# Kernel tuning notes

Hardware: AMD Instinct MI355X
Metric: run time of the kernel (lower is better)

The kernel has to match this reference:

```python
import jax, jax.numpy as jnp
import numpy as np

LN_EPS = 1e-5
ALPHA_Q = 1.0

def _ln(t, g, b):
    mu = jnp.mean(t, -1, keepdims=True)
    var = jnp.var(t, -1, keepdims=True)
    return (t - mu) / jnp.sqrt(var + LN_EPS) * g + b

def _mlp(t, w1, b1, w2, b2):
    h = jax.nn.gelu(t @ w1.T + b1, approximate=False)
    return h @ w2.T + b2

def setup_inputs() -> dict:
    key = jax.random.key(0)
    B, N, L, E, H, D = 2, 2048, 2048, 1024, 16, 4
    ks = jax.random.split(key, 40)
    rn = lambda i, shape, sc: jax.random.normal(ks[i], shape, jnp.float32) * sc
    inp = {}
    inp['x'] = rn(0, (B, N, E), 1.0)
    inp['xp'] = jax.random.uniform(ks[1], (B, N, D), jnp.float32)
    inp['y'] = rn(2, (B, L, E), 1.0)
    inp['yp'] = jax.random.uniform(ks[3], (B, L, D), jnp.float32)
    inp['attn_mask'] = jax.random.uniform(ks[4], (1, 1, N, L), jnp.float32)
    # PositionEncoder params (torch Linear convention: weight [out,in])
    inp['p_w1'] = rn(5, (E, D), 1.0 / D)
    inp['p_b1'] = jax.random.uniform(ks[6], (E,), jnp.float32, 0.0, np.pi)
    inp['p_w2'] = rn(7, (E, D), 1.0 / D)
    inp['p_b2'] = jax.random.uniform(ks[8], (E,), jnp.float32, 0.0, np.pi)
    # QueryEncoder: LayerNorm + mlp1 + mlp2 (mlp0 is dead code in the source)
    inp['q_ln_g'] = jnp.ones((E,), jnp.float32); inp['q_ln_b'] = jnp.zeros((E,), jnp.float32)
    inp['q_m1_w1'] = rn(9, (2 * E, E), 0.02); inp['q_m1_b1'] = jnp.zeros((2 * E,), jnp.float32)
    inp['q_m1_w2'] = rn(10, (E, 2 * E), 0.02); inp['q_m1_b2'] = jnp.zeros((E,), jnp.float32)
    inp['q_m2_w1'] = rn(11, (2 * E, E), 0.02); inp['q_m2_b1'] = jnp.zeros((2 * E,), jnp.float32)
    inp['q_m2_w2'] = rn(12, (E, 2 * E), 0.02); inp['q_m2_b2'] = jnp.zeros((E,), jnp.float32)
    # KeyEncoder: LayerNorm + mlp1 (mlp0 dead code)
    inp['k_ln_g'] = jnp.ones((E,), jnp.float32); inp['k_ln_b'] = jnp.zeros((E,), jnp.float32)
    inp['k_m1_w1'] = rn(13, (2 * E, E), 0.02); inp['k_m1_b1'] = jnp.zeros((2 * E,), jnp.float32)
    inp['k_m1_w2'] = rn(14, (E, 2 * E), 0.02); inp['k_m1_b2'] = jnp.zeros((E,), jnp.float32)
    # V: LayerNorm + Linear
    inp['v_ln_g'] = jnp.ones((E,), jnp.float32); inp['v_ln_b'] = jnp.zeros((E,), jnp.float32)
    inp['v_w'] = rn(15, (E, E), 0.02); inp['v_b'] = jnp.zeros((E,), jnp.float32)
    # output projections
    inp['proj1_w'] = rn(16, (E, E), 0.02); inp['proj1_b'] = jnp.zeros((E,), jnp.float32)
    inp['proj2_w'] = rn(17, (E, D * H), 0.02); inp['proj2_b'] = jnp.zeros((E,), jnp.float32)
    return inp

def reference(x, xp, y, yp, attn_mask, p_w1, p_b1, p_w2, p_b2,
              q_ln_g, q_ln_b, q_m1_w1, q_m1_b1, q_m1_w2, q_m1_b2,
              q_m2_w1, q_m2_b1, q_m2_w2, q_m2_b2,
              k_ln_g, k_ln_b, k_m1_w1, k_m1_b1, k_m1_w2, k_m1_b2,
              v_ln_g, v_ln_b, v_w, v_b, proj1_w, proj1_b, proj2_w, proj2_b):
    B, N, E = x.shape
    L = y.shape[1]
    D = xp.shape[2]
    H = proj2_w.shape[1] // D
    C = E // H
    # PositionEncoder: query side with bias, key side without bias
    pxt = ALPHA_Q * xp
    xp1 = pxt @ p_w1.T + p_b1            # [B,N,E]
    xp2 = pxt @ p_w2.T + p_b2
    pyt = ALPHA_Q * yp
    yp1 = pyt @ p_w1.T                   # [B,L,E], no bias
    yp2 = pyt @ p_w2.T
    rh = lambda t: t.reshape(t.shape[0], -1, H, C)
    # QueryEncoder
    xn = _ln(x, q_ln_g, q_ln_b)
    x1 = _mlp(xn, q_m1_w1, q_m1_b1, q_m1_w2, q_m1_b2)
    x2 = _mlp(xn, q_m2_w1, q_m2_b1, q_m2_w2, q_m2_b2)
    q = jnp.concatenate([rh(x1 * jnp.cos(xp1)), rh(x1 * jnp.sin(xp1)),
                         rh(x2 * jnp.cos(xp2)), rh(x2 * jnp.sin(xp2))], axis=-1)  # [B,N,H,4C]
    # KeyEncoder (note: second cos/sin block is the raw position code)
    yn = _ln(y, k_ln_g, k_ln_b)
    y1 = _mlp(yn, k_m1_w1, k_m1_b1, k_m1_w2, k_m1_b2)
    k = jnp.concatenate([rh(y1 * jnp.cos(yp1)), rh(y1 * jnp.sin(yp1)),
                         rh(jnp.cos(yp2)), rh(jnp.sin(yp2))], axis=-1)            # [B,L,H,4C]
    scale = (4 * C) ** (-0.5)
    attn = jax.nn.softmax(jnp.einsum('bnhd,blhd->bhnl', q, k) * scale, axis=-1)
    # masked renormalization (mask applied AFTER softmax)
    eps = min(1e-8, 1.0 / L)
    attn = attn * attn_mask
    attn = attn / (jnp.sum(attn, axis=-1, keepdims=True) + eps)
    # values
    v = (_ln(y, v_ln_g, v_ln_b) @ v_w.T + v_b).reshape(B, L, H, C)
    out1 = jnp.einsum('bhnl,blhc->bnhc', attn, v).reshape(B, N, E) @ proj1_w.T + proj1_b
    out2 = jnp.einsum('bhnl,bld->bnhd', attn, yp) - xp[:, :, None, :]             # [B,N,H,D]
    out2 = out2.reshape(B, N, H * D) @ proj2_w.T + proj2_b
    return (out1 + out2, attn, xp)
```

## Files before the change

### kernel.cpp

```cpp
#include <hip/hip_runtime.h>
#include <math.h>
#include <stdint.h>

#define DEV static __device__ __forceinline__

typedef __bf16 bf16x8 __attribute__((ext_vector_type(8)));
typedef __bf16 bf16x4v __attribute__((ext_vector_type(4)));
typedef float f32x4 __attribute__((ext_vector_type(4)));

constexpr int Nn = 2048, Ll = 2048, Ee = 1024, Hh = 16;
constexpr float SCALE = 0.0625f;

constexpr size_t OFF_XN   = 0;
constexpr size_t OFF_YNK  = 8388608;
constexpr size_t OFF_YNV  = 16777216;
constexpr size_t OFF_H12  = 25165824;
constexpr size_t OFF_H3   = 58720256;
constexpr size_t OFF_X1   = 75497472;
constexpr size_t OFF_X2   = 83886080;
constexpr size_t OFF_Y1   = 92274688;
constexpr size_t OFF_QWS  = 100663296;
constexpr size_t OFF_KWS  = 134217728;
constexpr size_t OFF_VWS  = 167772160;
constexpr size_t OFF_DNV  = 176160768;
constexpr size_t OFF_YPT  = 176422912;
constexpr size_t OFF_MSK  = 176685056;
constexpr size_t OFF_AVZ  = 185073664;
constexpr size_t OFF_W1122= 193986560;
constexpr size_t OFF_W12  = 202375168;
constexpr size_t OFF_W22  = 206569472;
constexpr size_t OFF_WK1  = 210763776;
constexpr size_t OFF_WK2  = 214958080;
constexpr size_t OFF_WV   = 219152384;
constexpr size_t OFF_WP   = 221249536;
constexpr size_t OFF_EM   = 223477760;

DEV void gl2l(const void* g, void* l) {
  __builtin_amdgcn_global_load_lds((const __attribute__((address_space(1))) void*)g,
                                   (__attribute__((address_space(3))) void*)l, 16, 0, 0);
}

DEV float gelu_f(float v) {
  float x = v * 0.70710678118654752f;
  float ax = fabsf(x);
  float t = 1.f / fmaf(0.3275911f, ax, 1.f);
  float y = t * fmaf(t, fmaf(t, fmaf(t, fmaf(t, 1.061405429f, -1.453152027f),
                                     1.421413741f), -0.284496736f), 0.254829592f);
  float er = 1.f - y * __expf(-x * x);
  er = (x < 0.f) ? -er : er;
  return 0.5f * v * (1.f + er);
}

__launch_bounds__(256)
__global__ void prep_all(const float* __restrict__ s0, const float* __restrict__ s1,
                         const float* __restrict__ s2, const float* __restrict__ s3,
                         const float* __restrict__ s4, const float* __restrict__ s5,
                         const float* __restrict__ s6,
                         __bf16* __restrict__ d0, __bf16* __restrict__ d1,
                         __bf16* __restrict__ d2, __bf16* __restrict__ d3,
                         __bf16* __restrict__ d4, __bf16* __restrict__ d5,
                         __bf16* __restrict__ d6,
                         const float* __restrict__ pw1, const float* __restrict__ pw2,
                         __bf16* __restrict__ wp,
                         const float* __restrict__ mask, __bf16* __restrict__ mb,
                         const float* __restrict__ yp, __bf16* __restrict__ ypT) {
  int u = blockIdx.x * 256 + threadIdx.x;
  if (u < 3407872) {
    int seg = u >> 19, r = u & 524287;
    const float* s; __bf16* d;
    if      (seg == 0) { s = s0; d = d0; }
    else if (seg == 1) { s = s1; d = d1; }
    else if (seg == 2) { s = s2; d = d2; }
    else if (seg == 3) { s = s3; d = d3; }
    else if (seg == 4) { s = s4; d = d4; }
    else if (seg == 5) { s = s5; d = d5; }
    else               { s = s6; d = d6; }
    float4 v = ((const float4*)s)[r];
    bf16x4v o; o[0]=(__bf16)v.x; o[1]=(__bf16)v.y; o[2]=(__bf16)v.z; o[3]=(__bf16)v.w;
    ((bf16x4v*)d)[r] = o;
  } else if (u < 3686400) {
    int p = u - 3407872;
    int row = p / 272, c4 = p - row * 272;
    float4 v = (c4 < 256) ? ((const float4*)pw1)[row * 256 + c4]
                          : ((const float4*)pw2)[row * 16 + (c4 - 256)];
    bf16x4v o; o[0]=(__bf16)v.x; o[1]=(__bf16)v.y; o[2]=(__bf16)v.z; o[3]=(__bf16)v.w;
    *(bf16x4v*)(wp + (size_t)row * 1088 + (c4 << 2)) = o;
  } else if (u < 4734976) {
    int q = u - 3686400;
    float4 v = ((const float4*)mask)[q];
    bf16x4v o; o[0]=(__bf16)v.x; o[1]=(__bf16)v.y; o[2]=(__bf16)v.z; o[3]=(__bf16)v.w;
    ((bf16x4v*)mb)[q] = o;
  } else {
    int t0 = (u - 4734976) << 2;
    #pragma unroll
    for (int k = 0; k < 4; k++) {
      int i = t0 + k;
      int b = i >> 13, d = (i >> 11) & 3, l = i & 2047;
      ypT[i] = (__bf16)yp[(((size_t)b << 11) + l) * 4 + d];
    }
  }
}

__launch_bounds__(256)
__global__ void ln_all(const float* __restrict__ x, const float* __restrict__ y,
                       const float* __restrict__ qg, const float* __restrict__ qb,
                       const float* __restrict__ kg, const float* __restrict__ kb,
                       const float* __restrict__ vg, const float* __restrict__ vb,
                       __bf16* __restrict__ xn, __bf16* __restrict__ ynk,
                       __bf16* __restrict__ ynv) {
  const int t = blockIdx.x, tid = threadIdx.x;
  const bool isx = t < 4096;
  const int row = isx ? t : t - 4096;
  const float* src = (isx ? x : y) + (size_t)row * Ee;
  const float4 v = ((const float4*)src)[tid];
  float s = v.x + v.y + v.z + v.w;
  float q = v.x*v.x + v.y*v.y + v.z*v.z + v.w*v.w;
  #pragma unroll
  for (int o = 32; o > 0; o >>= 1) { s += __shfl_down(s, o); q += __shfl_down(q, o); }
  __shared__ float ls[4], lq[4];
  if ((tid & 63) == 0) { ls[tid >> 6] = s; lq[tid >> 6] = q; }
  __syncthreads();
  s = ls[0] + ls[1] + ls[2] + ls[3];
  q = lq[0] + lq[1] + lq[2] + lq[3];
  const float mu = s * (1.f / Ee);
  const float rstd = rsqrtf(q * (1.f / Ee) - mu * mu + 1e-5f);
  const int e0 = tid << 2;
  float h0 = (v.x - mu) * rstd, h1 = (v.y - mu) * rstd,
        h2 = (v.z - mu) * rstd, h3 = (v.w - mu) * rstd;
  if (isx) {
    bf16x4v o;
    o[0] = (__bf16)(h0 * qg[e0]   + qb[e0]);
    o[1] = (__bf16)(h1 * qg[e0+1] + qb[e0+1]);
    o[2] = (__bf16)(h2 * qg[e0+2] + qb[e0+2]);
    o[3] = (__bf16)(h3 * qg[e0+3] + qb[e0+3]);
    *(bf16x4v*)(xn + (size_t)row * Ee + e0) = o;
  } else {
    bf16x4v ok, ov;
    ok[0] = (__bf16)(h0 * kg[e0]   + kb[e0]);
    ok[1] = (__bf16)(h1 * kg[e0+1] + kb[e0+1]);
    ok[2] = (__bf16)(h2 * kg[e0+2] + kb[e0+2]);
    ok[3] = (__bf16)(h3 * kg[e0+3] + kb[e0+3]);
    ov[0] = (__bf16)(h0 * vg[e0]   + vb[e0]);
    ov[1] = (__bf16)(h1 * vg[e0+1] + vb[e0+1]);
    ov[2] = (__bf16)(h2 * vg[e0+2] + vb[e0+2]);
    ov[3] = (__bf16)(h3 * vg[e0+3] + vb[e0+3]);
    *(bf16x4v*)(ynk + (size_t)row * Ee + e0) = ok;
    *(bf16x4v*)(ynv + (size_t)row * Ee + e0) = ov;
  }
}

#define GEMM256_CORE(A_, lda_, W_, ldw_, K_)                                          \
  const int w = tid >> 6, lane = tid & 63, g = lane >> 4, li = lane & 15;             \
  const int wm = (w >> 2) << 7, wn = (w & 3) << 6;                                    \
  f32x4 acc[8][4];                                                                    \
  _Pragma("unroll")                                                                   \
  for (int i = 0; i < 8; i++)                                                         \
    _Pragma("unroll")                                                                 \
    for (int j = 0; j < 4; j++) acc[i][j] = (f32x4)0.f;                               \
  auto stage = [&](int buf, int kt) {                                                 \
    const int col0 = kt << 5;                                                         \
    _Pragma("unroll")                                                                 \
    for (int jj = 0; jj < 2; jj++) {                                                  \
      int c = (jj << 9) + tid;                                                        \
      int row = c >> 2, sl = c & 3;                                                   \
      int col = col0 + ((sl ^ (row & 3)) << 3);                                       \
      gl2l(A_ + (size_t)(m0 + row) * lda_ + col, As[buf] + ((c - lane) << 3));        \
      gl2l(W_ + (size_t)(n0 + row) * ldw_ + col, Bs[buf] + ((c - lane) << 3));        \
    }                                                                                 \
  };                                                                                  \
  const int NT = (K_) >> 5;                                                           \
  stage(0, 0);                                                                        \
  __syncthreads();                                                                    \
  for (int kt = 0; kt < NT; kt++) {                                                   \
    const int cur = kt & 1;                                                           \
    if (kt + 1 < NT) stage(cur ^ 1, kt + 1);                                          \
    bf16x8 af[8], bw[4];                                                              \
    _Pragma("unroll")                                                                 \
    for (int i = 0; i < 8; i++) {                                                     \
      int ra = wm + (i << 4) + li;                                                    \
      af[i] = *(const bf16x8*)(As[cur] + ra * 32 + ((g ^ (ra & 3)) << 3));            \
    }                                                                                 \
    _Pragma("unroll")                                                                 \
    for (int j = 0; j < 4; j++) {                                                     \
      int rb = wn + (j << 4) + li;                                                    \
      bw[j] = *(const bf16x8*)(Bs[cur] + rb * 32 + ((g ^ (rb & 3)) << 3));            \
    }                                                                                 \
    _Pragma("unroll")                                                                 \
    for (int i = 0; i < 8; i++)                                                       \
      _Pragma("unroll")                                                               \
      for (int j = 0; j < 4; j++)                                                     \
        acc[i][j] = __builtin_amdgcn_mfma_f32_16x16x32_bf16(af[i], bw[j], acc[i][j], 0, 0, 0); \
    __syncthreads();                                                                  \
  }

__launch_bounds__(512, 2)
__global__ void gemm_mlp1(const __bf16* __restrict__ xn, const __bf16* __restrict__ ynk,
                          const __bf16* __restrict__ w1122, const __bf16* __restrict__ wk1,
                          const float* __restrict__ qb1, const float* __restrict__ qb2,
                          const float* __restrict__ kb1,
                          __bf16* __restrict__ h12, __bf16* __restrict__ h3) {
  __shared__ __align__(16) __bf16 As[2][256 * 32];
  __shared__ __align__(16) __bf16 Bs[2][256 * 32];
  const int tid = threadIdx.x, bid = blockIdx.x;
  const bool seg1 = bid >= 256;
  const __bf16* A; const __bf16* W; __bf16* out; int m0, n0, ldc;
  if (!seg1) { A = xn;  W = w1122; out = h12; ldc = 4096; m0 = (bid >> 4) << 8; n0 = (bid & 15) << 8; }
  else { int rr = bid - 256; A = ynk; W = wk1; out = h3; ldc = 2048; m0 = (rr >> 3) << 8; n0 = (rr & 7) << 8; }
  GEMM256_CORE(A, 1024, W, 1024, 1024)
  #pragma unroll
  for (int j = 0; j < 4; j++) {
    int n = n0 + wn + (j << 4) + li;
    float bias = seg1 ? kb1[n] : ((n < 2048) ? qb1[n] : qb2[n - 2048]);
    #pragma unroll
    for (int i = 0; i < 8; i++) {
      #pragma unroll
      for (int r = 0; r < 4; r++) {
        int m = m0 + wm + (i << 4) + (g << 2) + r;
        out[(size_t)m * ldc + n] = (__bf16)gelu_f(acc[i][j][r] + bias);
      }
    }
  }
}

__launch_bounds__(512, 2)
__global__ void gemm_mlp2(const __bf16* __restrict__ h12, const __bf16* __restrict__ h3,
                          const __bf16* __restrict__ ynv,
                          const __bf16* __restrict__ w12, const __bf16* __restrict__ w22,
                          const __bf16* __restrict__ wk2, const __bf16* __restrict__ wv,
                          const float* __restrict__ bx1, const float* __restrict__ bx2,
                          const float* __restrict__ by1, const float* __restrict__ bv,
                          __bf16* __restrict__ x1, __bf16* __restrict__ x2,
                          __bf16* __restrict__ y1, __bf16* __restrict__ vT) {
  __shared__ __align__(16) __bf16 As[2][256 * 32];
  __shared__ __align__(16) __bf16 Bs[2][256 * 32];
  const int tid = threadIdx.x, bid = blockIdx.x;
  const int seg = bid >> 6, rr = bid & 63;
  const int m0 = (rr >> 2) << 8, n0 = (rr & 3) << 8;
  const __bf16* A; const __bf16* W; const float* bias; __bf16* out; int lda, K;
  if      (seg == 0) { A = h12;        lda = 4096; W = w12; bias = bx1; out = x1; K = 2048; }
  else if (seg == 1) { A = h12 + 2048; lda = 4096; W = w22; bias = bx2; out = x2; K = 2048; }
  else if (seg == 2) { A = h3;         lda = 2048; W = wk2; bias = by1; out = y1; K = 2048; }
  else               { A = ynv;        lda = 1024; W = wv;  bias = bv;  out = vT; K = 1024; }
  GEMM256_CORE(A, lda, W, K, K)
  #pragma unroll
  for (int j = 0; j < 4; j++) {
    int n = n0 + wn + (j << 4) + li;
    float bs = bias[n];
    #pragma unroll
    for (int i = 0; i < 8; i++) {
      #pragma unroll
      for (int r = 0; r < 4; r++) {
        int m = m0 + wm + (i << 4) + (g << 2) + r;
        float v = acc[i][j][r] + bs;
        if (seg == 3) {
          int bb = m >> 11, l = m & 2047, hh = n >> 6, cc = n & 63;
          vT[(((size_t)(bb * Hh + hh) * 64 + cc) << 11) + l] = (__bf16)v;
        } else {
          out[(size_t)m * 1024 + n] = (__bf16)v;
        }
      }
    }
  }
}

__launch_bounds__(256)
__global__ void gemm_proj(const __bf16* __restrict__ A, const __bf16* __restrict__ W,
                          const float* __restrict__ bias1, const float* __restrict__ bias2,
                          float* __restrict__ out) {
  constexpr int N = 1024, K = 1088;
  __shared__ __align__(16) __bf16 As[2][128 * 32];
  __shared__ __align__(16) __bf16 Bs[2][64 * 32];
  const int tid = threadIdx.x;
  const int w = tid >> 6, lane = tid & 63, g = lane >> 4, li = lane & 15;
  const int bt = blockIdx.x >> 4;
  const int m0 = bt << 7, n0 = (blockIdx.x & 15) << 6;
  const int wm = (w >> 1) << 6, wn = (w & 1) << 5;
  f32x4 acc[4][2];
  #pragma unroll
  for (int i = 0; i < 4; i++) { acc[i][0] = (f32x4)0.f; acc[i][1] = (f32x4)0.f; }
  auto stage = [&](int buf, int kt) {
    const int col0 = kt << 5;
    #pragma unroll
    for (int j = 0; j < 2; j++) {
      int c = (j << 8) + tid;
      int row = c >> 2, sl = c & 3;
      int col = col0 + ((sl ^ (row & 3)) << 3);
      gl2l(A + (size_t)(m0 + row) * K + col, As[buf] + ((c - lane) << 3));
    }
    {
      int c = tid;
      int row = c >> 2, sl = c & 3;
      int col = col0 + ((sl ^ (row & 3)) << 3);
      gl2l(W + (size_t)(n0 + row) * K + col, Bs[buf] + ((c - lane) << 3));
    }
  };
  const int NT = K >> 5;
  stage(0, 0);
  __syncthreads();
  for (int kt = 0; kt < NT; kt++) {
    const int cur = kt & 1;
    if (kt + 1 < NT) stage(cur ^ 1, kt + 1);
    bf16x8 af[4], bw[2];
    #pragma unroll
    for (int i = 0; i < 4; i++) {
      int ra = wm + (i << 4) + li;
      af[i] = *(const bf16x8*)(As[cur] + ra * 32 + ((g ^ (ra & 3)) << 3));
    }
    #pragma unroll
    for (int j = 0; j < 2; j++) {
      int rb = wn + (j << 4) + li;
      bw[j] = *(const bf16x8*)(Bs[cur] + rb * 32 + ((g ^ (rb & 3)) << 3));
    }
    #pragma unroll
    for (int i = 0; i < 4; i++)
      #pragma unroll
      for (int j = 0; j < 2; j++)
        acc[i][j] = __builtin_amdgcn_mfma_f32_16x16x32_bf16(af[i], bw[j], acc[i][j], 0, 0, 0);
    __syncthreads();
  }
  #pragma unroll
  for (int j = 0; j < 2; j++) {
    int n = n0 + wn + (j << 4) + li;
    float bias = bias1[n] + bias2[n];
    #pragma unroll
    for (int i = 0; i < 4; i++) {
      #pragma unroll
      for (int r = 0; r < 4; r++) {
        int m = m0 + wm + (i << 4) + (g << 2) + r;
        out[(size_t)m * N + n] = acc[i][j][r] + bias;
      }
    }
  }
}

__launch_bounds__(256)
__global__ void build_qk(const __bf16* __restrict__ x1, const __bf16* __restrict__ x2,
                         const float* __restrict__ xp,
                         const __bf16* __restrict__ y1, const float* __restrict__ yp,
                         const float* __restrict__ pw1, const float* __restrict__ pb1,
                         const float* __restrict__ pw2, const float* __restrict__ pb2,
                         __bf16* __restrict__ q_ws, __bf16* __restrict__ k_ws) {
  const bool isq = blockIdx.x < 2048;
  const int bid = isq ? blockIdx.x : blockIdx.x - 2048;
  const int t = (bid << 1) + (threadIdx.x >> 7);
  const int tl = threadIdx.x & 127;
  const int b = t >> 11, n = t & 2047;
  const int hh = tl >> 3, ch = tl & 7;
  const int e0 = (hh << 6) + (ch << 3);
  const float* pos = isq ? xp : yp;
  const float p0 = pos[(size_t)t*4], p1 = pos[(size_t)t*4+1],
              p2 = pos[(size_t)t*4+2], p3 = pos[(size_t)t*4+3];
  bf16x8 o0, o1, o2, o3;
  if (isq) {
    bf16x8 v1 = *(const bf16x8*)(x1 + (size_t)t * Ee + e0);
    bf16x8 v2 = *(const bf16x8*)(x2 + (size_t)t * Ee + e0);
    #pragma unroll
    for (int sub = 0; sub < 8; sub++) {
      int e = e0 + sub;
      float a1 = pw1[e*4]*p0 + pw1[e*4+1]*p1 + pw1[e*4+2]*p2 + pw1[e*4+3]*p3 + pb1[e];
      float a2 = pw2[e*4]*p0 + pw2[e*4+1]*p1 + pw2[e*4+2]*p2 + pw2[e*4+3]*p3 + pb2[e];
      float s1, c1, s2, c2;
      __sincosf(a1, &s1, &c1); __sincosf(a2, &s2, &c2);
      float xv1 = (float)v1[sub], xv2 = (float)v2[sub];
      o0[sub] = (__bf16)(xv1 * c1); o1[sub] = (__bf16)(xv1 * s1);
      o2[sub] = (__bf16)(xv2 * c2); o3[sub] = (__bf16)(xv2 * s2);
    }
  } else {
    bf16x8 v1 = *(const bf16x8*)(y1 + (size_t)t * Ee + e0);
    #pragma unroll
    for (int sub = 0; sub < 8; sub++) {
      int e = e0 + sub;
      float a1 = pw1[e*4]*p0 + pw1[e*4+1]*p1 + pw1[e*4+2]*p2 + pw1[e*4+3]*p3;
      float a2 = pw2[e*4]*p0 + pw2[e*4+1]*p1 + pw2[e*4+2]*p2 + pw2[e*4+3]*p3;
      float s1, c1, s2, c2;
      __sincosf(a1, &s1, &c1); __sincosf(a2, &s2, &c2);
      float yv = (float)v1[sub];
      o0[sub] = (__bf16)(yv * c1); o1[sub] = (__bf16)(yv * s1);
      o2[sub] = (__bf16)c2;        o3[sub] = (__bf16)s2;
    }
  }
  const int k = n & 7, bc = ch ^ k;
  __bf16* base = (isq ? q_ws : k_ws) + ((((size_t)b * Hh + hh) * Nn + n) << 8);
  *(bf16x8*)(base + ((bc          ) << 3)) = o0;
  *(bf16x8*)(base + (((8  ^ k) ^ ch) << 3)) = o1;
  *(bf16x8*)(base + (((16 ^ k) ^ ch) << 3)) = o2;
  *(bf16x8*)(base + (((24 ^ k) ^ ch) << 3)) = o3;
}

__launch_bounds__(512, 1)
__global__ void attn_fused(const __bf16* __restrict__ q_ws, const __bf16* __restrict__ k_ws,
                           const __bf16* __restrict__ vT_ws, const __bf16* __restrict__ ypT_g,
                           const __bf16* __restrict__ mask_bf, const float* __restrict__ xp,
                           __bf16* __restrict__ em_g, float* __restrict__ dinv_g,
                           __bf16* __restrict__ avz) {
  __shared__ __align__(16) __bf16 kq[2][32 * 256];
  __shared__ __align__(16) __bf16 ms[2][256 * 32];
  __shared__ __align__(16) __bf16 vt[2][64 * 40];
  __shared__ __align__(16) __bf16 pT[256 * 40];
  __shared__ __align__(16) __bf16 ypl[2][16 * 40];
  const int tid = threadIdx.x, w = tid >> 6, lane = tid & 63, g = lane >> 4, li = lane & 15;
  const int logical = ((blockIdx.x & 7) << 5) + (blockIdx.x >> 3);
  const int bh = logical >> 3, nt = logical & 7;
  const int b = bh >> 4, h = bh & 15;
  const int n0 = nt << 8;
  const __bf16* qb = q_ws + (((size_t)bh * Nn + n0) << 8);
  const __bf16* kb = k_ws + (((size_t)bh * Ll) << 8);
  const __bf16* vb = vT_ws + ((size_t)bh << 17);
  const __bf16* yb = ypT_g + ((size_t)b << 13);
  const __bf16* mb = mask_bf + ((size_t)n0 << 11);

  bf16x8 aq[2][8];
  #pragma unroll
  for (int rf = 0; rf < 2; rf++) {
    const int nloc = (w << 5) + (rf << 4) + li;
    #pragma unroll
    for (int s = 0; s < 8; s++)
      aq[rf][s] = *(const bf16x8*)(qb + ((size_t)nloc << 8) + ((((s << 2) + g) ^ (nloc & 7)) << 3));
  }
  for (int i = tid; i < 960; i += 512) {
    int buf = i / 480, idx = i - buf * 480;
    ypl[buf][160 + idx] = (__bf16)0.f;
  }
  {
    const int vc = tid >> 3, vl = (tid & 7) << 2;
    bf16x4v vreg = *(const bf16x4v*)(vb + ((size_t)vc << 11) + vl);
    bf16x4v ypreg;
    if (tid < 32) ypreg = *(const bf16x4v*)(yb + ((size_t)(tid >> 3) << 11) + ((tid & 7) << 2));
    #pragma unroll
    for (int j = 0; j < 2; j++) {
      int c = (j << 9) + tid;
      gl2l(kb + (size_t)(c >> 5) * 256 + ((c & 31) << 3), kq[0] + ((c - lane) << 3));
      gl2l(mb + (size_t)(c >> 2) * 2048 + ((c & 3) << 3), ms[0] + ((c - lane) << 3));
    }
    *(bf16x4v*)(vt[0] + vc * 40 + vl) = vreg;
    if (tid < 32) *(bf16x4v*)(ypl[0] + (tid >> 3) * 40 + ((tid & 7) << 2)) = ypreg;
  }
  __syncthreads();

  float se[2][4], te[2][4];
  f32x4 accv[2][4], accp[2];
  #pragma unroll
  for (int rf = 0; rf < 2; rf++) {
    #pragma unroll
    for (int r = 0; r < 4; r++) { se[rf][r] = 0.f; te[rf][r] = 0.f; }
    #pragma unroll
    for (int cb = 0; cb < 4; cb++) accv[rf][cb] = (f32x4)0.f;
    accp[rf] = (f32x4)0.f;
  }

  for (int t = 0; t < 64; ++t) {
    const int l0 = t << 5, cur = t & 1, nxt = cur ^ 1;
    const bool more = (t < 63);
    bf16x4v vreg, ypreg;
    if (more) {
      const int l1 = l0 + 32;
      vreg = *(const bf16x4v*)(vb + ((size_t)(tid >> 3) << 11) + l1 + ((tid & 7) << 2));
      if (tid < 32) ypreg = *(const bf16x4v*)(yb + ((size_t)(tid >> 3) << 11) + l1 + ((tid & 7) << 2));
      #pragma unroll
      for (int j = 0; j < 2; j++) {
        int c = (j << 9) + tid;
        gl2l(kb + (size_t)(l1 + (c >> 5)) * 256 + ((c & 31) << 3), kq[nxt] + ((c - lane) << 3));
        gl2l(mb + (size_t)(c >> 2) * 2048 + l1 + ((c & 3) << 3), ms[nxt] + ((c - lane) << 3));
      }
    }
    f32x4 Cs[2][2];
    Cs[0][0] = (f32x4)0.f; Cs[0][1] = (f32x4)0.f; Cs[1][0] = (f32x4)0.f; Cs[1][1] = (f32x4)0.f;
    #pragma unroll
    for (int lb = 0; lb < 2; lb++) {
      const int kr = (lb << 4) + li;
      #pragma unroll
      for (int s = 0; s < 8; s++) {
        bf16x8 bk = *(const bf16x8*)(kq[cur] + kr * 256 + ((((s << 2) + g) ^ (kr & 7)) << 3));
        Cs[0][lb] = __builtin_amdgcn_mfma_f32_16x16x32_bf16(aq[0][s], bk, Cs[0][lb], 0, 0, 0);
        Cs[1][lb] = __builtin_amdgcn_mfma_f32_16x16x32_bf16(aq[1][s], bk, Cs[1][lb], 0, 0, 0);
      }
    }
    #pragma unroll
    for (int rf = 0; rf < 2; rf++) {
      #pragma unroll
      for (int lb = 0; lb < 2; lb++) {
        #pragma unroll
        for (int r = 0; r < 4; r++) {
          const int row = (w << 5) + (rf << 4) + (g << 2) + r;
          float e = __expf(Cs[rf][lb][r] * SCALE);
          float mkv = (float)ms[cur][row * 32 + (lb << 4) + li];
          float em = e * mkv;
          se[rf][r] += e; te[rf][r] += em;
          pT[row * 40 + (lb << 4) + li] = (__bf16)em;
        }
      }
    }
    asm volatile("s_waitcnt lgkmcnt(0)" ::: "memory");
    __builtin_amdgcn_sched_barrier(0);
    #pragma unroll
    for (int j = 0; j < 2; j++) {
      int q = (j << 6) + lane;
      int row = q >> 2, ch = q & 3;
      bf16x8 pv = *(const bf16x8*)(pT + ((w << 5) + row) * 40 + (ch << 3));
      *(bf16x8*)(em_g + ((size_t)bh << 22) + ((size_t)(n0 + (w << 5) + row) << 11) + l0 + (ch << 3)) = pv;
    }
    bf16x8 vv[4];
    #pragma unroll
    for (int cb = 0; cb < 4; cb++)
      vv[cb] = *(const bf16x8*)(vt[cur] + ((cb << 4) + li) * 40 + (g << 3));
    bf16x8 yy = *(const bf16x8*)(ypl[cur] + li * 40 + (g << 3));
    #pragma unroll
    for (int rf = 0; rf < 2; rf++) {
      bf16x8 pa = *(const bf16x8*)(pT + ((w << 5) + (rf << 4) + li) * 40 + (g << 3));
      #pragma unroll
      for (int cb = 0; cb < 4; cb++)
        accv[rf][cb] = __builtin_amdgcn_mfma_f32_16x16x32_bf16(pa, vv[cb], accv[rf][cb], 0, 0, 0);
      accp[rf] = __builtin_amdgcn_mfma_f32_16x16x32_bf16(pa, yy, accp[rf], 0, 0, 0);
    }
    if (more) {
      *(bf16x4v*)(vt[nxt] + (tid >> 3) * 40 + ((tid & 7) << 2)) = vreg;
      if (tid < 32) *(bf16x4v*)(ypl[nxt] + (tid >> 3) * 40 + ((tid & 7) << 2)) = ypreg;
    }
    __syncthreads();
  }

  #pragma unroll
  for (int rf = 0; rf < 2; rf++) {
    #pragma unroll
    for (int r = 0; r < 4; r++) {
      float s = se[rf][r], tt = te[rf][r];
      #pragma unroll
      for (int o = 1; o < 16; o <<= 1) { s += __shfl_xor(s, o); tt += __shfl_xor(tt, o); }
      float dinv = 1.f / (tt + 1e-8f * s);
      const int n = n0 + (w << 5) + (rf << 4) + (g << 2) + r;
      if (li == 0) dinv_g[((size_t)bh << 11) + n] = dinv;
      #pragma unroll
      for (int cb = 0; cb < 4; cb++)
        avz[((size_t)b * Nn + n) * 1088 + (h << 6) + (cb << 4) + li] = (__bf16)(accv[rf][cb][r] * dinv);
      if (li < 4) {
        float z = accp[rf][r] * dinv - xp[(((size_t)b * Nn + n) << 2) + li];
        avz[((size_t)b * Nn + n) * 1088 + 1024 + (h << 2) + li] = (__bf16)z;
      }
    }
  }
}

__launch_bounds__(256)
__global__ void attn_fin(const __bf16* __restrict__ em_g, const float* __restrict__ dinv_g,
                         float* __restrict__ attn_out,
                         const float* __restrict__ xp, float* __restrict__ xp_out) {
  if (blockIdx.x < 64) {
    int idx = blockIdx.x * 256 + threadIdx.x;
    ((float4*)xp_out)[idx] = ((const float4*)xp)[idx];
  }
  for (size_t i8 = blockIdx.x * 256ul + threadIdx.x; i8 < 16777216ul; i8 += 524288ul) {
    bf16x8 v = ((const bf16x8*)em_g)[i8];
    float dv = dinv_g[i8 >> 8];
    float4 o0, o1;
    o0.x = (float)v[0] * dv; o0.y = (float)v[1] * dv; o0.z = (float)v[2] * dv; o0.w = (float)v[3] * dv;
    o1.x = (float)v[4] * dv; o1.y = (float)v[5] * dv; o1.z = (float)v[6] * dv; o1.w = (float)v[7] * dv;
    ((float4*)attn_out)[i8 * 2]     = o0;
    ((float4*)attn_out)[i8 * 2 + 1] = o1;
  }
}

extern "C" void kernel_launch(void* const* d_in, const int* in_sizes, int n_in,
                              void* d_out, int out_size, void* d_ws, size_t ws_size,
                              hipStream_t stream) {
  (void)in_sizes; (void)n_in; (void)out_size; (void)ws_size;
  const float* x       = (const float*)d_in[0];
  const float* xp      = (const float*)d_in[1];
  const float* y       = (const float*)d_in[2];
  const float* yp      = (const float*)d_in[3];
  const float* mask    = (const float*)d_in[4];
  const float* p_w1    = (const float*)d_in[5];
  const float* p_b1    = (const float*)d_in[6];
  const float* p_w2    = (const float*)d_in[7];
  const float* p_b2    = (const float*)d_in[8];
  const float* q_ln_g  = (const float*)d_in[9];
  const float* q_ln_b  = (const float*)d_in[10];
  const float* q_m1_w1 = (const float*)d_in[11];
  const float* q_m1_b1 = (const float*)d_in[12];
  const float* q_m1_w2 = (const float*)d_in[13];
  const float* q_m1_b2 = (const float*)d_in[14];
  const float* q_m2_w1 = (const float*)d_in[15];
  const float* q_m2_b1 = (const float*)d_in[16];
  const float* q_m2_w2 = (const float*)d_in[17];
  const float* q_m2_b2 = (const float*)d_in[18];
  const float* k_ln_g  = (const float*)d_in[19];
  const float* k_ln_b  = (const float*)d_in[20];
  const float* k_m1_w1 = (const float*)d_in[21];
  const float* k_m1_b1 = (const float*)d_in[22];
  const float* k_m1_w2 = (const float*)d_in[23];
  const float* k_m1_b2 = (const float*)d_in[24];
  const float* v_ln_g  = (const float*)d_in[25];
  const float* v_ln_b  = (const float*)d_in[26];
  const float* v_w     = (const float*)d_in[27];
  const float* v_b     = (const float*)d_in[28];
  const float* proj1_w = (const float*)d_in[29];
  const float* proj1_b = (const float*)d_in[30];
  const float* proj2_w = (const float*)d_in[31];
  const float* proj2_b = (const float*)d_in[32];

  char* ws = (char*)d_ws;
  __bf16* xn    = (__bf16*)(ws + OFF_XN);
  __bf16* ynk   = (__bf16*)(ws + OFF_YNK);
  __bf16* ynv   = (__bf16*)(ws + OFF_YNV);
  __bf16* h12   = (__bf16*)(ws + OFF_H12);
  __bf16* h3    = (__bf16*)(ws + OFF_H3);
  __bf16* x1    = (__bf16*)(ws + OFF_X1);
  __bf16* x2    = (__bf16*)(ws + OFF_X2);
  __bf16* y1    = (__bf16*)(ws + OFF_Y1);
  __bf16* q_ws  = (__bf16*)(ws + OFF_QWS);
  __bf16* k_ws  = (__bf16*)(ws + OFF_KWS);
  __bf16* vT_ws = (__bf16*)(ws + OFF_VWS);
  float*  dinv  = (float*)(ws + OFF_DNV);
  __bf16* ypT   = (__bf16*)(ws + OFF_YPT);
  __bf16* mskb  = (__bf16*)(ws + OFF_MSK);
  __bf16* avz   = (__bf16*)(ws + OFF_AVZ);
  __bf16* w1122 = (__bf16*)(ws + OFF_W1122);
  __bf16* w12   = (__bf16*)(ws + OFF_W12);
  __bf16* w22   = (__bf16*)(ws + OFF_W22);
  __bf16* wk1   = (__bf16*)(ws + OFF_WK1);
  __bf16* wk2   = (__bf16*)(ws + OFF_WK2);
  __bf16* wv    = (__bf16*)(ws + OFF_WV);
  __bf16* wp    = (__bf16*)(ws + OFF_WP);
  __bf16* em    = (__bf16*)(ws + OFF_EM);

  float* out0     = (float*)d_out;
  float* attn_out = out0 + (size_t)4194304;
  float* xp_out   = out0 + (size_t)138412032;

  prep_all<<<18512, 256, 0, stream>>>(q_m1_w1, q_m2_w1, q_m1_w2, q_m2_w2, k_m1_w1, k_m1_w2, v_w,
                                      w1122, w1122 + 2097152, w12, w22, wk1, wk2, wv,
                                      proj1_w, proj2_w, wp, mask, mskb, yp, ypT);
  ln_all<<<8192, 256, 0, stream>>>(x, y, q_ln_g, q_ln_b, k_ln_g, k_ln_b, v_ln_g, v_ln_b,
                                   xn, ynk, ynv);
  gemm_mlp1<<<384, 512, 0, stream>>>(xn, ynk, w1122, wk1, q_m1_b1, q_m2_b1, k_m1_b1, h12, h3);
  gemm_mlp2<<<256, 512, 0, stream>>>(h12, h3, ynv, w12, w22, wk2, wv,
                                     q_m1_b2, q_m2_b2, k_m1_b2, v_b, x1, x2, y1, vT_ws);
  build_qk<<<4096, 256, 0, stream>>>(x1, x2, xp, y1, yp, p_w1, p_b1, p_w2, p_b2, q_ws, k_ws);
  attn_fused<<<256, 512, 0, stream>>>(q_ws, k_ws, vT_ws, ypT, mskb, xp, em, dinv, avz);
  attn_fin<<<2048, 256, 0, stream>>>(em, dinv, attn_out, xp, xp_out);
  gemm_proj<<<512, 256, 0, stream>>>(avz, wp, proj1_b, proj2_b, out0);
}
```

Baseline: 732.2 us.

## Merge attn finalize with output projection and relax GEMM loop synchronization

Measured after the change: 733.8 us. No clear change (+0.2%).

```diff
diff --git a/kernel.cpp b/kernel.cpp
--- a/kernel.cpp
+++ b/kernel.cpp
@@ -170,10 +170,16 @@
   };                                                                                  \
   const int NT = (K_) >> 5;                                                           \
   stage(0, 0);                                                                        \
-  __syncthreads();                                                                    \
   for (int kt = 0; kt < NT; kt++) {                                                   \
     const int cur = kt & 1;                                                           \
-    if (kt + 1 < NT) stage(cur ^ 1, kt + 1);                                          \
+    if (kt + 1 < NT) {                                                                \
+      stage(cur ^ 1, kt + 1);                                                         \
+      asm volatile("s_waitcnt vmcnt(4)" ::: "memory");                                \
+    } else {                                                                          \
+      asm volatile("s_waitcnt vmcnt(0)" ::: "memory");                                \
+    }                                                                                 \
+    __builtin_amdgcn_s_barrier();                                                     \
+    __builtin_amdgcn_sched_barrier(0);                                                \
     bf16x8 af[8], bw[4];                                                              \
     _Pragma("unroll")                                                                 \
     for (int i = 0; i < 8; i++) {                                                     \
@@ -190,7 +196,9 @@
       _Pragma("unroll")                                                               \
       for (int j = 0; j < 4; j++)                                                     \
         acc[i][j] = __builtin_amdgcn_mfma_f32_16x16x32_bf16(af[i], bw[j], acc[i][j], 0, 0, 0); \
-    __syncthreads();                                                                  \
+    asm volatile("s_waitcnt lgkmcnt(0)" ::: "memory");                                \
+    __builtin_amdgcn_sched_barrier(0);                                                \
+    __builtin_amdgcn_s_barrier();                                                     \
   }
 
 __launch_bounds__(512, 2)
@@ -258,76 +266,6 @@
         } else {
           out[(size_t)m * 1024 + n] = (__bf16)v;
         }
-      }
-    }
-  }
-}
-
-__launch_bounds__(256)
-__global__ void gemm_proj(const __bf16* __restrict__ A, const __bf16* __restrict__ W,
-                          const float* __restrict__ bias1, const float* __restrict__ bias2,
-                          float* __restrict__ out) {
-  constexpr int N = 1024, K = 1088;
-  __shared__ __align__(16) __bf16 As[2][128 * 32];
-  __shared__ __align__(16) __bf16 Bs[2][64 * 32];
-  const int tid = threadIdx.x;
-  const int w = tid >> 6, lane = tid & 63, g = lane >> 4, li = lane & 15;
-  const int bt = blockIdx.x >> 4;
-  const int m0 = bt << 7, n0 = (blockIdx.x & 15) << 6;
-  const int wm = (w >> 1) << 6, wn = (w & 1) << 5;
-  f32x4 acc[4][2];
-  #pragma unroll
-  for (int i = 0; i < 4; i++) { acc[i][0] = (f32x4)0.f; acc[i][1] = (f32x4)0.f; }
-  auto stage = [&](int buf, int kt) {
-    const int col0 = kt << 5;
-    #pragma unroll
-    for (int j = 0; j < 2; j++) {
-      int c = (j << 8) + tid;
-      int row = c >> 2, sl = c & 3;
-      int col = col0 + ((sl ^ (row & 3)) << 3);
-      gl2l(A + (size_t)(m0 + row) * K + col, As[buf] + ((c - lane) << 3));
-    }
-    {
-      int c = tid;
-      int row = c >> 2, sl = c & 3;
-      int col = col0 + ((sl ^ (row & 3)) << 3);
-      gl2l(W + (size_t)(n0 + row) * K + col, Bs[buf] + ((c - lane) << 3));
-    }
-  };
-  const int NT = K >> 5;
-  stage(0, 0);
-  __syncthreads();
-  for (int kt = 0; kt < NT; kt++) {
-    const int cur = kt & 1;
-    if (kt + 1 < NT) stage(cur ^ 1, kt + 1);
-    bf16x8 af[4], bw[2];
-    #pragma unroll
-    for (int i = 0; i < 4; i++) {
-      int ra = wm + (i << 4) + li;
-      af[i] = *(const bf16x8*)(As[cur] + ra * 32 + ((g ^ (ra & 3)) << 3));
-    }
-    #pragma unroll
-    for (int j = 0; j < 2; j++) {
-      int rb = wn + (j << 4) + li;
-      bw[j] = *(const bf16x8*)(Bs[cur] + rb * 32 + ((g ^ (rb & 3)) << 3));
-    }
-    #pragma unroll
-    for (int i = 0; i < 4; i++)
-      #pragma unroll
-      for (int j = 0; j < 2; j++)
-        acc[i][j] = __builtin_amdgcn_mfma_f32_16x16x32_bf16(af[i], bw[j], acc[i][j], 0, 0, 0);
-    __syncthreads();
-  }
-  #pragma unroll
-  for (int j = 0; j < 2; j++) {
-    int n = n0 + wn + (j << 4) + li;
-    float bias = bias1[n] + bias2[n];
-    #pragma unroll
-    for (int i = 0; i < 4; i++) {
-      #pragma unroll
-      for (int r = 0; r < 4; r++) {
-        int m = m0 + wm + (i << 4) + (g << 2) + r;
-        out[(size_t)m * N + n] = acc[i][j][r] + bias;
       }
     }
   }
@@ -541,21 +479,100 @@
 }
 
 __launch_bounds__(256)
-__global__ void attn_fin(const __bf16* __restrict__ em_g, const float* __restrict__ dinv_g,
+__global__ void fin_proj(const __bf16* __restrict__ A, const __bf16* __restrict__ W,
+                         const float* __restrict__ bias1, const float* __restrict__ bias2,
+                         float* __restrict__ out,
+                         const __bf16* __restrict__ em_g, const float* __restrict__ dinv_g,
                          float* __restrict__ attn_out,
                          const float* __restrict__ xp, float* __restrict__ xp_out) {
-  if (blockIdx.x < 64) {
-    int idx = blockIdx.x * 256 + threadIdx.x;
-    ((float4*)xp_out)[idx] = ((const float4*)xp)[idx];
-  }
-  for (size_t i8 = blockIdx.x * 256ul + threadIdx.x; i8 < 16777216ul; i8 += 524288ul) {
-    bf16x8 v = ((const bf16x8*)em_g)[i8];
-    float dv = dinv_g[i8 >> 8];
-    float4 o0, o1;
-    o0.x = (float)v[0] * dv; o0.y = (float)v[1] * dv; o0.z = (float)v[2] * dv; o0.w = (float)v[3] * dv;
-    o1.x = (float)v[4] * dv; o1.y = (float)v[5] * dv; o1.z = (float)v[6] * dv; o1.w = (float)v[7] * dv;
-    ((float4*)attn_out)[i8 * 2]     = o0;
-    ((float4*)attn_out)[i8 * 2 + 1] = o1;
+  constexpr int N = 1024, K = 1088;
+  __shared__ __align__(16) __bf16 As[2][128 * 32];
+  __shared__ __align__(16) __bf16 Bs[2][64 * 32];
+  const int tid = threadIdx.x;
+  if (blockIdx.x >= 512) {
+    const int sbid = blockIdx.x - 512;
+    if (sbid < 64) {
+      int idx = sbid * 256 + tid;
+      ((float4*)xp_out)[idx] = ((const float4*)xp)[idx];
+    }
+    for (size_t i8 = sbid * 256ul + tid; i8 < 16777216ul; i8 += 524288ul) {
+      bf16x8 v = ((const bf16x8*)em_g)[i8];
+      float dv = dinv_g[i8 >> 8];
+      float4 o0, o1;
+      o0.x = (float)v[0] * dv; o0.y = (float)v[1] * dv; o0.z = (float)v[2] * dv; o0.w = (float)v[3] * dv;
+      o1.x = (float)v[4] * dv; o1.y = (float)v[5] * dv; o1.z = (float)v[6] * dv; o1.w = (float)v[7] * dv;
+      ((float4*)attn_out)[i8 * 2]     = o0;
+      ((float4*)attn_out)[i8 * 2 + 1] = o1;
+    }
+    return;
+  }
+  const int w = tid >> 6, lane = tid & 63, g = lane >> 4, li = lane & 15;
+  const int bt = blockIdx.x >> 4;
+  const int m0 = bt << 7, n0 = (blockIdx.x & 15) << 6;
+  const int wm = (w >> 1) << 6, wn = (w & 1) << 5;
+  f32x4 acc[4][2];
+  #pragma unroll
+  for (int i = 0; i < 4; i++) { acc[i][0] = (f32x4)0.f; acc[i][1] = (f32x4)0.f; }
+  auto stage = [&](int buf, int kt) {
+    const int col0 = kt << 5;
+    #pragma unroll
+    for (int j = 0; j < 2; j++) {
+      int c = (j << 8) + tid;
+      int row = c >> 2, sl = c & 3;
+      int col = col0 + ((sl ^ (row & 3)) << 3);
+      gl2l(A + (size_t)(m0 + row) * K + col, As[buf] + ((c - lane) << 3));
+    }
+    {
+      int c = tid;
+      int row = c >> 2, sl = c & 3;
+      int col = col0 + ((sl ^ (row & 3)) << 3);
+      gl2l(W + (size_t)(n0 + row) * K + col, Bs[buf] + ((c - lane) << 3));
+    }
+  };
+  const int NT = K >> 5;
+  stage(0, 0);
+  for (int kt = 0; kt < NT; kt++) {
+    const int cur = kt & 1;
+    if (kt + 1 < NT) {
+      stage(cur ^ 1, kt + 1);
+      asm volatile("s_waitcnt vmcnt(3)" ::: "memory");
+    } else {
+      asm volatile("s_waitcnt vmcnt(0)" ::: "memory");
+    }
+    __builtin_amdgcn_s_barrier();
+    __builtin_amdgcn_sched_barrier(0);
+    bf16x8 af[4], bw[2];
+    #pragma unroll
+    for (int i = 0; i < 4; i++) {
+      int ra = wm + (i << 4) + li;
+      af[i] = *(const bf16x8*)(As[cur] + ra * 32 + ((g ^ (ra & 3)) << 3));
+    }
+    #pragma unroll
+    for (int j = 0; j < 2; j++) {
+      int rb = wn + (j << 4) + li;
+      bw[j] = *(const bf16x8*)(Bs[cur] + rb * 32 + ((g ^ (rb & 3)) << 3));
+    }
+    #pragma unroll
+    for (int i = 0; i < 4; i++)
+      #pragma unroll
+      for (int j = 0; j < 2; j++)
+        acc[i][j] = __builtin_amdgcn_mfma_f32_16x16x32_bf16(af[i], bw[j], acc[i][j], 0, 0, 0);
+    asm volatile("s_waitcnt lgkmcnt(0)" ::: "memory");
+    __builtin_amdgcn_sched_barrier(0);
+    __builtin_amdgcn_s_barrier();
+  }
+  #pragma unroll
+  for (int j = 0; j < 2; j++) {
+    int n = n0 + wn + (j << 4) + li;
+    float bias = bias1[n] + bias2[n];
+    #pragma unroll
+    for (int i = 0; i < 4; i++) {
+      #pragma unroll
+      for (int r = 0; r < 4; r++) {
+        int m = m0 + wm + (i << 4) + (g << 2) + r;
+        out[(size_t)m * N + n] = acc[i][j][r] + bias;
+      }
+    }
   }
 }
 
@@ -636,6 +653,6 @@
                                      q_m1_b2, q_m2_b2, k_m1_b2, v_b, x1, x2, y1, vT_ws);
   build_qk<<<4096, 256, 0, stream>>>(x1, x2, xp, y1, yp, p_w1, p_b1, p_w2, p_b2, q_ws, k_ws);
   attn_fused<<<256, 512, 0, stream>>>(q_ws, k_ws, vT_ws, ypT, mskb, xp, em, dinv, avz);
-  attn_fin<<<2048, 256, 0, stream>>>(em, dinv, attn_out, xp, xp_out);
-  gemm_proj<<<512, 256, 0, stream>>>(avz, wp, proj1_b, proj2_b, out0);
-}
+  fin_proj<<<2560, 256, 0, stream>>>(avz, wp, proj1_b, proj2_b, out0,
+                                     em, dinv, attn_out, xp, xp_out);
+}
```
